# Performance work log

Hardware: AMD Instinct MI355X
Metric: run time of the kernel (lower is better)

Reference implementation:

```python
import jax, jax.numpy as jnp
import numpy as np

B = 16384          # batch size
NNZ_PER = 32       # active features per board (max pieces)
FT_OUT = 1024
BUCKETS = 8
FEAT = 768


def setup_inputs() -> dict:
    key = jax.random.key(0)
    k1, k2, k3, k4, k5, k6, k7 = jax.random.split(key, 7)
    nnz = B * NNZ_PER
    b_idx = jnp.repeat(jnp.arange(B, dtype=jnp.int64), NNZ_PER)
    stm_f = jax.random.randint(k1, (nnz,), 0, FEAT, dtype=jnp.int64)
    nstm_f = jax.random.randint(k2, (nnz,), 0, FEAT, dtype=jnp.int64)
    stm_indices = jnp.stack([b_idx, stm_f], axis=1)
    nstm_indices = jnp.stack([b_idx, nstm_f], axis=1)
    values = jnp.ones((nnz,), dtype=jnp.float32)
    buckets = jax.random.randint(k3, (B,), 0, BUCKETS, dtype=jnp.int64)
    ft_w = jax.random.normal(k4, (FT_OUT, FEAT), dtype=jnp.float32) * 0.02
    ft_b = jax.random.normal(k5, (FT_OUT,), dtype=jnp.float32) * 0.02
    out_w = jax.random.normal(k6, (BUCKETS, 2 * FT_OUT), dtype=jnp.float32) * 0.02
    out_b = jax.random.normal(k7, (BUCKETS,), dtype=jnp.float32) * 0.02
    return {"stm_indices": stm_indices, "nstm_indices": nstm_indices,
            "values": values, "buckets": buckets, "size": B,
            "ft_w": ft_w, "ft_b": ft_b, "out_w": out_w, "out_b": out_b}


def _to_dense(indices, values, size):
    # sparse_coo_tensor(...).to_dense(): duplicate coords sum
    board = jnp.zeros((size, FEAT), dtype=values.dtype)
    return board.at[indices[:, 0], indices[:, 1]].add(values)


def reference(stm_indices, nstm_indices, values, buckets, size, ft_w, ft_b, out_w, out_b):
    board_stm = _to_dense(stm_indices, values, size)    # [B, 768]
    board_nstm = _to_dense(nstm_indices, values, size)  # [B, 768]
    stm_ft = board_stm @ ft_w.T + ft_b                  # [B, FT_OUT]
    nstm_ft = board_nstm @ ft_w.T + ft_b
    hidden = jnp.clip(jnp.concatenate([stm_ft, nstm_ft], axis=1), 0.0, 1.0)  # [B, 2*FT_OUT]
    l1 = hidden @ out_w.T + out_b                       # [B, BUCKETS]
    # per-row bucket gather == view(-1,1)[buckets + arange(B)*bucket_count]
    l1_out = jnp.take_along_axis(l1, buckets[:, None], axis=1)  # [B, 1]
    return jax.nn.sigmoid(l1_out)
```

## Files before the change

kernel.cpp:

```cpp
#include <hip/hip_runtime.h>
#include <hip/hip_bf16.h>
#include <math.h>

#define B_SZ    16384
#define NNZ     32
#define FT_OUT  1024
#define FEAT    768
#define BUCKETS 8
#define M_TOT   (2 * B_SZ)

typedef __bf16 bf16x8 __attribute__((ext_vector_type(8)));
typedef float  f32x4  __attribute__((ext_vector_type(4)));
typedef __attribute__((ext_vector_type(8))) short short8;

__device__ __forceinline__ unsigned short f2b(float f) {
    return __bfloat16_as_ushort(__float2bfloat16(f));
}
__device__ __forceinline__ float b2f(unsigned short u) {
    union { unsigned int i; float f; } x; x.i = ((unsigned int)u) << 16; return x.f;
}
__device__ __forceinline__ void gld_lds16(const void* g, void* l) {
    __builtin_amdgcn_global_load_lds(
        (const __attribute__((address_space(1))) unsigned int*)g,
        (__attribute__((address_space(3))) unsigned int*)l, 16, 0, 0);
}

#define PREP_BUILD  8192
#define PREP_CVT    12
#define PREP_ZERO   16

__global__ __launch_bounds__(256) void prep(
    const int*    __restrict__ stm_idx, const int* __restrict__ nstm_idx,
    const float*  __restrict__ values,
    const float2* __restrict__ ftw2,    unsigned int* __restrict__ Wout,
    unsigned short* __restrict__ A,     float* __restrict__ logit) {
    const int bid = blockIdx.x;
    if (bid < PREP_BUILD) {
        __shared__ float rowbuf[4][FEAT];
        const int wave = threadIdx.x >> 6, lane = threadIdx.x & 63;
        const int m = bid * 4 + wave;
        const int board = m & (B_SZ - 1);
        const int* idx = (m >= B_SZ) ? nstm_idx : stm_idx;
        float* rb = rowbuf[wave];
#pragma unroll
        for (int i = 0; i < FEAT / 64; ++i) rb[i * 64 + lane] = 0.0f;
        __syncthreads();
        if (lane < NNZ) {
            int   f = idx[(board * NNZ + lane) * 2 + 1];
            float v = values[board * NNZ + lane];
            atomicAdd(&rb[f], v);
        }
        __syncthreads();
        unsigned int* dst = (unsigned int*)(A + (long)m * FEAT);
#pragma unroll
        for (int i = 0; i < FEAT / 128; ++i) {
            int e = i * 64 + lane;
            unsigned int lo = f2b(rb[2 * e]), hi = f2b(rb[2 * e + 1]);
            dst[e] = lo | (hi << 16);
        }
    } else if (bid < PREP_BUILD + PREP_CVT) {
        int tid = (bid - PREP_BUILD) * 256 + threadIdx.x;
        for (int i = tid; i < FT_OUT * FEAT / 2; i += PREP_CVT * 256) {
            float2 v = ftw2[i];
            Wout[i] = (unsigned int)f2b(v.x) | ((unsigned int)f2b(v.y) << 16);
        }
    } else {
        int tid = (bid - PREP_BUILD - PREP_CVT) * 256 + threadIdx.x;
        for (int i = tid; i < B_SZ; i += PREP_ZERO * 256) logit[i] = 0.0f;
    }
}

#define BM 256
#define BN 256
#define BK 64
#define NKT (FEAT / BK)

__global__ __launch_bounds__(512, 1) void gemm_head(
    const unsigned short* __restrict__ A,
    const unsigned short* __restrict__ W,
    const float* __restrict__ ft_b,
    const float* __restrict__ out_w,
    const int*   __restrict__ buckets,
    float*       __restrict__ logit)
{
    __shared__ unsigned short smA[2][BM * BK];
    __shared__ unsigned short smB[2][BN * BK];
    const int wv = threadIdx.x >> 6, lane = threadIdx.x & 63;
    const int wm = wv >> 2, wn = wv & 3;

    const int bid = blockIdx.x;
    const int wg  = (bid & 7) * 64 + (bid >> 3);
    const int tileM = (wg >> 2) * BM;
    const int tileN = (wg & 3) * BN;

    f32x4 acc[8][4] = {};

    const int srow  = wv * 32 + (lane >> 3);
    const int skoff = ((lane & 7) ^ (lane >> 3)) * 8;

#define STAGE(buf, kt)                                                        \
    {                                                                         \
        const int k0_ = (kt) * BK;                                            \
        _Pragma("unroll")                                                     \
        for (int q = 0; q < 4; ++q) {                                         \
            gld_lds16(A + (long)(tileM + srow + q * 8) * FEAT + k0_ + skoff,  \
                      &smA[buf][(wv * 32 + q * 8) * BK]);                     \
            gld_lds16(W + (long)(tileN + srow + q * 8) * FEAT + k0_ + skoff,  \
                      &smB[buf][(wv * 32 + q * 8) * BK]);                     \
        }                                                                     \
    }

    const int cx = lane & 7;
    const int rq = lane >> 4;

    STAGE(0, 0);

    for (int t = 0; t < NKT; ++t) {
        const int b = t & 1;
        if (t + 1 < NKT) {
            STAGE(b ^ 1, t + 1);
            asm volatile("s_waitcnt vmcnt(8)" ::: "memory");
        } else {
            asm volatile("s_waitcnt vmcnt(0)" ::: "memory");
        }
        __builtin_amdgcn_s_barrier();
        asm volatile("" ::: "memory");
#pragma unroll
        for (int ki = 0; ki < 2; ++ki) {
            const int koff = ((ki * 4 + rq) ^ cx) * 8;
            bf16x8 af[8], bfr[4];
#pragma unroll
            for (int f = 0; f < 8; ++f)
                af[f] = *(const bf16x8*)(&smA[b][(wm * 128 + f * 16 + (lane & 15)) * BK + koff]);
#pragma unroll
            for (int f = 0; f < 4; ++f)
                bfr[f] = *(const bf16x8*)(&smB[b][(wn * 64 + f * 16 + (lane & 15)) * BK + koff]);
            __builtin_amdgcn_s_setprio(1);
#pragma unroll
            for (int mf = 0; mf < 8; ++mf)
#pragma unroll
                for (int nf = 0; nf < 4; ++nf)
                    acc[mf][nf] = __builtin_amdgcn_mfma_f32_16x16x32_bf16(
                        af[mf], bfr[nf], acc[mf][nf], 0, 0, 0);
            __builtin_amdgcn_s_setprio(0);
        }
        asm volatile("" ::: "memory");
        __builtin_amdgcn_s_barrier();
    }

    float ftb[4]; int cols[4];
#pragma unroll
    for (int nf = 0; nf < 4; ++nf) {
        cols[nf] = tileN + wn * 64 + nf * 16 + (lane & 15);
        ftb[nf]  = ft_b[cols[nf]];
    }
    const int sideoff = (tileM >= B_SZ) ? FT_OUT : 0;

#pragma unroll
    for (int mf = 0; mf < 8; ++mf) {
#pragma unroll
        for (int r = 0; r < 4; ++r) {
            int mloc  = wm * 128 + mf * 16 + rq * 4 + r;
            int board = (tileM + mloc) & (B_SZ - 1);
            int bkt   = buckets[board];
            const float* ow = out_w + bkt * (2 * FT_OUT) + sideoff;
            float p = 0.0f;
#pragma unroll
            for (int nf = 0; nf < 4; ++nf) {
                float h = acc[mf][nf][r] + ftb[nf];
                h = fminf(fmaxf(h, 0.0f), 1.0f);
                p += h * ow[cols[nf]];
            }
            p += __shfl_xor(p, 1);
            p += __shfl_xor(p, 2);
            p += __shfl_xor(p, 4);
            p += __shfl_xor(p, 8);
            if ((lane & 15) == 0) atomicAdd(logit + board, p);
        }
    }
#undef STAGE
}

__global__ __launch_bounds__(256) void finish(const float* __restrict__ logit,
                                              const int* __restrict__ buckets,
                                              const float* __restrict__ out_b,
                                              float* __restrict__ out) {
    int b = blockIdx.x * 256 + threadIdx.x;
    float l = logit[b] + out_b[buckets[b]];
    out[b] = 1.0f / (1.0f + expf(-l));
}

__global__ __launch_bounds__(256) void transpose_ftw_bf16(
    const float* __restrict__ ft_w, unsigned short* __restrict__ ftT) {
    __shared__ float tile[32][33];
    const int fo = blockIdx.x * 32, oo = blockIdx.y * 32;
    const int tx = threadIdx.x & 31, ty = threadIdx.x >> 5;
#pragma unroll
    for (int i = 0; i < 4; ++i)
        tile[ty + 8 * i][tx] = ft_w[(oo + ty + 8 * i) * FEAT + fo + tx];
    __syncthreads();
#pragma unroll
    for (int i = 0; i < 4; ++i)
        ftT[(fo + ty + 8 * i) * FT_OUT + oo + tx] = f2b(tile[tx][ty + 8 * i]);
}

__global__ __launch_bounds__(256) void nn_fwd(
    const int* __restrict__ stm_idx, const int* __restrict__ nstm_idx,
    const float* __restrict__ values, const int* __restrict__ buckets,
    const unsigned short* __restrict__ ftT, const float* __restrict__ ft_b,
    const float* __restrict__ out_w, const float* __restrict__ out_b,
    float* __restrict__ out) {
    const int wave = threadIdx.x >> 6, lane = threadIdx.x & 63;
    const int b = __builtin_amdgcn_readfirstlane(blockIdx.x * 4 + wave);
    float acc_s[2][8], acc_n[2][8];
#pragma unroll
    for (int c = 0; c < 2; ++c) {
        const float4* fb = (const float4*)(ft_b + c * 512 + lane * 8);
        float4 b0 = fb[0], b1 = fb[1];
        float t[8] = {b0.x,b0.y,b0.z,b0.w,b1.x,b1.y,b1.z,b1.w};
#pragma unroll
        for (int j = 0; j < 8; ++j) { acc_s[c][j] = t[j]; acc_n[c][j] = t[j]; }
    }
    const int base = b * NNZ;
#pragma unroll 4
    for (int k = 0; k < NNZ; ++k) {
        const int fs = stm_idx[(base + k) * 2 + 1];
        const int fn = nstm_idx[(base + k) * 2 + 1];
        const float v = values[base + k];
        const unsigned short* cs = ftT + fs * FT_OUT;
        const unsigned short* cn = ftT + fn * FT_OUT;
#pragma unroll
        for (int c = 0; c < 2; ++c) {
            short8 ws = *(const short8*)(cs + c * 512 + lane * 8);
            short8 wn2 = *(const short8*)(cn + c * 512 + lane * 8);
#pragma unroll
            for (int j = 0; j < 8; ++j) {
                acc_s[c][j] = fmaf(v, b2f((unsigned short)ws[j]), acc_s[c][j]);
                acc_n[c][j] = fmaf(v, b2f((unsigned short)wn2[j]), acc_n[c][j]);
            }
        }
    }
    const int bkt = __builtin_amdgcn_readfirstlane(buckets[b]);
    const float* ow = out_w + bkt * (2 * FT_OUT);
    float part = 0.0f;
#pragma unroll
    for (int c = 0; c < 2; ++c) {
        const float4* ps = (const float4*)(ow + c * 512 + lane * 8);
        const float4* pn = (const float4*)(ow + FT_OUT + c * 512 + lane * 8);
        float4 s0 = ps[0], s1 = ps[1], n0 = pn[0], n1 = pn[1];
        float sw[8] = {s0.x,s0.y,s0.z,s0.w,s1.x,s1.y,s1.z,s1.w};
        float nw[8] = {n0.x,n0.y,n0.z,n0.w,n1.x,n1.y,n1.z,n1.w};
#pragma unroll
        for (int j = 0; j < 8; ++j) {
            part += fminf(fmaxf(acc_s[c][j], 0.f), 1.f) * sw[j];
            part += fminf(fmaxf(acc_n[c][j], 0.f), 1.f) * nw[j];
        }
    }
#pragma unroll
    for (int off = 32; off >= 1; off >>= 1) part += __shfl_xor(part, off);
    if (lane == 0) out[b] = 1.0f / (1.0f + expf(-(part + out_b[bkt])));
}

extern "C" void kernel_launch(void* const* d_in, const int* in_sizes, int n_in,
                              void* d_out, int out_size, void* d_ws, size_t ws_size,
                              hipStream_t stream) {
    const int*   stm_idx  = (const int*)  d_in[0];
    const int*   nstm_idx = (const int*)  d_in[1];
    const float* values   = (const float*)d_in[2];
    const int*   buckets  = (const int*)  d_in[3];
    const float* ft_w     = (const float*)d_in[5];
    const float* ft_b     = (const float*)d_in[6];
    const float* out_w    = (const float*)d_in[7];
    const float* out_b    = (const float*)d_in[8];
    float*       out      = (float*)d_out;

    const size_t szA = (size_t)M_TOT * FEAT * 2;
    const size_t szW = (size_t)FT_OUT * FEAT * 2;
    const size_t NEED = szA + szW + (size_t)B_SZ * 4;

    if (ws_size >= NEED) {
        unsigned short* A  = (unsigned short*)d_ws;
        unsigned short* W  = (unsigned short*)((char*)d_ws + szA);
        float*          lg = (float*)((char*)d_ws + szA + szW);

        prep<<<PREP_BUILD + PREP_CVT + PREP_ZERO, 256, 0, stream>>>(
            stm_idx, nstm_idx, values, (const float2*)ft_w, (unsigned int*)W,
            A, lg);
        gemm_head<<<(M_TOT / BM) * (FT_OUT / BN), 512, 0, stream>>>(
            A, W, ft_b, out_w, buckets, lg);
        finish<<<B_SZ / 256, 256, 0, stream>>>(lg, buckets, out_b, out);
    } else {
        unsigned short* ftT = (unsigned short*)d_ws;
        transpose_ftw_bf16<<<dim3(FEAT / 32, FT_OUT / 32), 256, 0, stream>>>(ft_w, ftT);
        nn_fwd<<<B_SZ / 4, 256, 0, stream>>>(stm_idx, nstm_idx, values, buckets,
                                             ftT, ft_b, out_w, out_b, out);
    }
}
```

Measured before the change: 188.3 us.

## Restructure GEMM main loop into four-phase half-tile pipeline with finer-grained staging

The GEMM k-loop is split into four phases, each handling half an M-fragment group and half a K-step. Each phase issues an asynchronous global-to-LDS load for a future tile half before its MFMA block, so loads overlap with compute at finer granularity. The LDS layout changes to 32-wide K sub-tiles with a new XOR swizzle, and register pressure drops because only 4 A fragments are held at a time. Separately, the prep weight-conversion path now launches one thread per element instead of 12 looping blocks. The extra barriers and hand-tuned vmcnt waits add synchronization overhead and raise the risk of ordering mistakes.

```diff
diff --git a/kernel.cpp b/kernel.cpp
--- a/kernel.cpp
+++ b/kernel.cpp
@@ -26,7 +26,7 @@
 }
 
 #define PREP_BUILD  8192
-#define PREP_CVT    12
+#define PREP_CVT    1536
 #define PREP_ZERO   16
 
 __global__ __launch_bounds__(256) void prep(
@@ -59,11 +59,9 @@
             dst[e] = lo | (hi << 16);
         }
     } else if (bid < PREP_BUILD + PREP_CVT) {
-        int tid = (bid - PREP_BUILD) * 256 + threadIdx.x;
-        for (int i = tid; i < FT_OUT * FEAT / 2; i += PREP_CVT * 256) {
-            float2 v = ftw2[i];
-            Wout[i] = (unsigned int)f2b(v.x) | ((unsigned int)f2b(v.y) << 16);
-        }
+        int i = (bid - PREP_BUILD) * 256 + threadIdx.x;
+        float2 v = ftw2[i];
+        Wout[i] = (unsigned int)f2b(v.x) | ((unsigned int)f2b(v.y) << 16);
     } else {
         int tid = (bid - PREP_BUILD - PREP_CVT) * 256 + threadIdx.x;
         for (int i = tid; i < B_SZ; i += PREP_ZERO * 256) logit[i] = 0.0f;
@@ -83,8 +81,8 @@
     const int*   __restrict__ buckets,
     float*       __restrict__ logit)
 {
-    __shared__ unsigned short smA[2][BM * BK];
-    __shared__ unsigned short smB[2][BN * BK];
+    __shared__ unsigned short smA[2 * 2 * 256 * 32];
+    __shared__ unsigned short smB[2 * 2 * 256 * 32];
     const int wv = threadIdx.x >> 6, lane = threadIdx.x & 63;
     const int wm = wv >> 2, wn = wv & 3;
 
@@ -95,63 +93,93 @@
 
     f32x4 acc[8][4] = {};
 
-    const int srow  = wv * 32 + (lane >> 3);
-    const int skoff = ((lane & 7) ^ (lane >> 3)) * 8;
-
-#define STAGE(buf, kt)                                                        \
-    {                                                                         \
-        const int k0_ = (kt) * BK;                                            \
+    const int l15       = lane & 15;
+    const int rq        = lane >> 4;
+    const int sRowOff   = lane >> 2;
+    const int sColChunk = ((lane & 3) ^ ((lane >> 3) & 3)) * 8;
+    const int rdChunk   = (rq ^ ((lane >> 1) & 3)) * 8;
+
+#define STAGE_HALF(sm, gsrc, gRowBase, TT, KI, DBUF)                          \
+    { _Pragma("unroll")                                                       \
+      for (int q_ = 0; q_ < 2; ++q_) {                                        \
+          const int rr_ = (q_ * 8 + wv) * 16;                                 \
+          gld_lds16(gsrc + (long)(gRowBase + rr_ + sRowOff) * FEAT            \
+                         + (TT) * BK + (KI) * 32 + sColChunk,                 \
+                    sm + (((DBUF) * 2 + (KI)) * 256 + rr_) * 32);             \
+      } }
+
+#define LDA(DBUF, KI, FROW) \
+    (*(const bf16x8*)(smA + ((((DBUF)*2+(KI))*256 + (FROW) + l15) * 32 + rdChunk)))
+#define LDB(DBUF, KI, FROW) \
+    (*(const bf16x8*)(smB + ((((DBUF)*2+(KI))*256 + (FROW) + l15) * 32 + rdChunk)))
+
+    STAGE_HALF(smB, W, tileN, 0, 0, 0); STAGE_HALF(smA, A, tileM, 0, 0, 0);
+    STAGE_HALF(smB, W, tileN, 0, 1, 0); STAGE_HALF(smA, A, tileM, 0, 1, 0);
+    STAGE_HALF(smB, W, tileN, 1, 0, 1); STAGE_HALF(smA, A, tileM, 1, 0, 1);
+    STAGE_HALF(smB, W, tileN, 1, 1, 1); STAGE_HALF(smA, A, tileM, 1, 1, 1);
+    asm volatile("s_waitcnt vmcnt(8)" ::: "memory");
+    __builtin_amdgcn_s_barrier();
+
+    bf16x8 af[4], bfr[4];
+
+#define MFMA16(G)                                                             \
+    __builtin_amdgcn_s_setprio(1);                                            \
+    _Pragma("unroll")                                                         \
+    for (int mf = 0; mf < 4; ++mf)                                            \
         _Pragma("unroll")                                                     \
-        for (int q = 0; q < 4; ++q) {                                         \
-            gld_lds16(A + (long)(tileM + srow + q * 8) * FEAT + k0_ + skoff,  \
-                      &smA[buf][(wv * 32 + q * 8) * BK]);                     \
-            gld_lds16(W + (long)(tileN + srow + q * 8) * FEAT + k0_ + skoff,  \
-                      &smB[buf][(wv * 32 + q * 8) * BK]);                     \
-        }                                                                     \
-    }
-
-    const int cx = lane & 7;
-    const int rq = lane >> 4;
-
-    STAGE(0, 0);
+        for (int nf = 0; nf < 4; ++nf)                                        \
+            acc[(G)*4+mf][nf] = __builtin_amdgcn_mfma_f32_16x16x32_bf16(      \
+                af[mf], bfr[nf], acc[(G)*4+mf][nf], 0, 0, 0);                 \
+    __builtin_amdgcn_s_setprio(0);
+
+#define PH_SYNC_IN                                                            \
+    __builtin_amdgcn_sched_barrier(0);                                        \
+    __builtin_amdgcn_s_barrier();                                             \
+    asm volatile("s_waitcnt lgkmcnt(0)" ::: "memory");                        \
+    __builtin_amdgcn_sched_barrier(0);
 
     for (int t = 0; t < NKT; ++t) {
-        const int b = t & 1;
-        if (t + 1 < NKT) {
-            STAGE(b ^ 1, t + 1);
-            asm volatile("s_waitcnt vmcnt(8)" ::: "memory");
-        } else {
-            asm volatile("s_waitcnt vmcnt(0)" ::: "memory");
-        }
+        const int c = t & 1;
+        if (t >= 1 && t + 1 < NKT) STAGE_HALF(smA, A, tileM, t + 1, 1, (t + 1) & 1);
+#pragma unroll
+        for (int nf = 0; nf < 4; ++nf) bfr[nf] = LDB(c, 0, wn * 64 + nf * 16);
+#pragma unroll
+        for (int mf = 0; mf < 4; ++mf) af[mf] = LDA(c, 0, wm * 128 + mf * 16);
+        PH_SYNC_IN
+        MFMA16(0)
+        __builtin_amdgcn_sched_barrier(0);
         __builtin_amdgcn_s_barrier();
-        asm volatile("" ::: "memory");
-#pragma unroll
-        for (int ki = 0; ki < 2; ++ki) {
-            const int koff = ((ki * 4 + rq) ^ cx) * 8;
-            bf16x8 af[8], bfr[4];
-#pragma unroll
-            for (int f = 0; f < 8; ++f)
-                af[f] = *(const bf16x8*)(&smA[b][(wm * 128 + f * 16 + (lane & 15)) * BK + koff]);
-#pragma unroll
-            for (int f = 0; f < 4; ++f)
-                bfr[f] = *(const bf16x8*)(&smB[b][(wn * 64 + f * 16 + (lane & 15)) * BK + koff]);
-            __builtin_amdgcn_s_setprio(1);
-#pragma unroll
-            for (int mf = 0; mf < 8; ++mf)
-#pragma unroll
-                for (int nf = 0; nf < 4; ++nf)
-                    acc[mf][nf] = __builtin_amdgcn_mfma_f32_16x16x32_bf16(
-                        af[mf], bfr[nf], acc[mf][nf], 0, 0, 0);
-            __builtin_amdgcn_s_setprio(0);
-        }
-        asm volatile("" ::: "memory");
+        if (t + 2 < NKT) STAGE_HALF(smB, W, tileN, t + 2, 0, c);
+#pragma unroll
+        for (int mf = 0; mf < 4; ++mf) af[mf] = LDA(c, 0, wm * 128 + 64 + mf * 16);
+        PH_SYNC_IN
+        MFMA16(1)
+        asm volatile("s_waitcnt vmcnt(10)" ::: "memory");
+        __builtin_amdgcn_sched_barrier(0);
         __builtin_amdgcn_s_barrier();
+        if (t + 2 < NKT) STAGE_HALF(smA, A, tileM, t + 2, 0, c);
+#pragma unroll
+        for (int nf = 0; nf < 4; ++nf) bfr[nf] = LDB(c, 1, wn * 64 + nf * 16);
+#pragma unroll
+        for (int mf = 0; mf < 4; ++mf) af[mf] = LDA(c, 1, wm * 128 + mf * 16);
+        PH_SYNC_IN
+        MFMA16(0)
+        __builtin_amdgcn_sched_barrier(0);
+        __builtin_amdgcn_s_barrier();
+        if (t + 2 < NKT) STAGE_HALF(smB, W, tileN, t + 2, 1, c);
+#pragma unroll
+        for (int mf = 0; mf < 4; ++mf) af[mf] = LDA(c, 1, wm * 128 + 64 + mf * 16);
+        PH_SYNC_IN
+        MFMA16(1)
+        asm volatile("s_waitcnt vmcnt(10)" ::: "memory");
+        __builtin_amdgcn_sched_barrier(0);
+        __builtin_amdgcn_s_barrier();
     }
 
     float ftb[4]; int cols[4];
 #pragma unroll
     for (int nf = 0; nf < 4; ++nf) {
-        cols[nf] = tileN + wn * 64 + nf * 16 + (lane & 15);
+        cols[nf] = tileN + wn * 64 + nf * 16 + l15;
         ftb[nf]  = ft_b[cols[nf]];
     }
     const int sideoff = (tileM >= B_SZ) ? FT_OUT : 0;
@@ -178,7 +206,11 @@
             if ((lane & 15) == 0) atomicAdd(logit + board, p);
         }
     }
-#undef STAGE
+#undef STAGE_HALF
+#undef LDA
+#undef LDB
+#undef MFMA16
+#undef PH_SYNC_IN
 }
 
 __global__ __launch_bounds__(256) void finish(const float* __restrict__ logit,
```

Result: faster. 177.1 us (-5.9%).
